# Kernel optimization log

Measured on AMD Instinct MI355X. Metric: run time of the kernel, lower is better.

The kernel has to match this reference:

```python
import jax, jax.numpy as jnp
import numpy as np

N, M, E, DIM, H = 50000, 50000, 640000, 128, 8
DH = DIM // H
EPS = 1e-5

def _prelu(x, alpha):
    return jnp.where(x >= 0, x, alpha * x)

def setup_inputs() -> dict:
    key0 = jax.random.key(0)
    ks = jax.random.split(key0, 12)
    s = 1.0 / np.sqrt(DIM)
    return {
        "query": jax.random.normal(ks[0], (N, DIM), jnp.float32),
        "key": jax.random.normal(ks[1], (M, DIM), jnp.float32),
        "value": jax.random.normal(ks[2], (M, DIM), jnp.float32),
        "query_idx": jax.random.randint(ks[3], (E,), 0, N),
        "key_idx": jax.random.randint(ks[4], (E,), 0, M),
        "Wq": jax.random.normal(ks[5], (DIM, DIM), jnp.float32) * s,
        "bq": jnp.zeros((DIM,), jnp.float32),
        "Wk": jax.random.normal(ks[6], (DIM, DIM), jnp.float32) * s,
        "bk": jnp.zeros((DIM,), jnp.float32),
        "Wv": jax.random.normal(ks[7], (DIM, DIM), jnp.float32) * s,
        "bv": jnp.zeros((DIM,), jnp.float32),
        "Wp": jax.random.normal(ks[8], (DIM, DIM), jnp.float32) * s,
        "bp": jnp.zeros((DIM,), jnp.float32),
        "a": jax.random.normal(ks[9], (1, H, DH), jnp.float32) * 0.1,
        "alpha": jnp.full((1,), 0.25, jnp.float32),
        "gamma": jnp.ones((DIM,), jnp.float32),
        "beta": jnp.zeros((DIM,), jnp.float32),
    }

def reference(query, key, value, query_idx, key_idx, Wq, bq, Wk, bk, Wv, bv, Wp, bp, a, alpha, gamma, beta):
    n = query.shape[0]
    # projections (node-level, then gather per edge; linear commutes with gather)
    Qq = query @ Wq + bq            # [N, DIM]
    Kq = query @ Wk + bk            # [N, DIM] (self-attn key)
    Kk = key @ Wk + bk              # [M, DIM]
    Vq = query @ Wv + bv            # [N, DIM]
    Vv = value @ Wv + bv            # [M, DIM]
    # self-attention score per query node: [N, H, 1]
    attn_qq = (a * _prelu(Qq + Kq, alpha).reshape(n, H, DH)).sum(-1, keepdims=True)
    # per-edge additive attention score: [E, H, 1]
    e_feat = _prelu(Qq[query_idx] + Kk[key_idx], alpha)
    attn_e = (a * e_feat.reshape(-1, H, DH)).sum(-1, keepdims=True)
    # stable softmax over irregular query groups (include self)
    max_attn = jax.lax.stop_gradient(attn_qq.at[query_idx].max(attn_e))
    exp_qq = jnp.exp(attn_qq - max_attn)                 # [N, H, 1]
    exp_e = jnp.exp(attn_e - max_attn[query_idx])        # [E, H, 1]
    denom = exp_qq.at[query_idx].add(exp_e)              # [N, H, 1]
    denom = jnp.where(denom == 0, 1.0, denom)
    # weighted value scatter-sum (value_idx == key_idx)
    msg = exp_qq * Vq.reshape(n, H, DH)
    msg = msg.at[query_idx].add(exp_e * Vv[key_idx].reshape(-1, H, DH))
    out = (msg / denom).reshape(n, DIM) @ Wp + bp
    res = query + out
    mu = res.mean(-1, keepdims=True)
    var = res.var(-1, keepdims=True)
    return gamma * (res - mu) / jnp.sqrt(var + EPS) + beta
```

## Files before the change

kernel.cpp:

```cpp
#include <hip/hip_runtime.h>
#include <math.h>

#define DIM 128
#define NH 8
#define LN_EPS 1e-5f
#define NEGINF -3.0e38f

using bf16x8 = __attribute__((ext_vector_type(8))) short;
using f32x4  = __attribute__((ext_vector_type(4))) float;

__device__ __forceinline__ float prelu_f(float x, float al) { return x >= 0.f ? x : al * x; }

__device__ __forceinline__ short f2bf(float f) {
    unsigned u = __float_as_uint(f);
    unsigned r = (u + 0x7fffu + ((u >> 16) & 1u)) >> 16;
    return (short)r;
}
__device__ __forceinline__ float bflo(unsigned u) { return __uint_as_float(u << 16); }
__device__ __forceinline__ float bfhi(unsigned u) { return __uint_as_float(u & 0xffff0000u); }

__device__ __forceinline__ unsigned cvt_pk_bf16(float lo, float hi) {
    unsigned r;
    asm("v_cvt_pk_bf16_f32 %0, %1, %2" : "=v"(r) : "v"(lo), "v"(hi));
    return r;
}

__device__ __forceinline__ float swz_xor1(float x) {
    return __int_as_float(__builtin_amdgcn_ds_swizzle(__float_as_int(x), 0x041F));
}
__device__ __forceinline__ float swz_xor2(float x) {
    return __int_as_float(__builtin_amdgcn_ds_swizzle(__float_as_int(x), 0x081F));
}
__device__ __forceinline__ float swz_xor16(float x) {
    return __int_as_float(__builtin_amdgcn_ds_swizzle(__float_as_int(x), 0x401F));
}
__device__ __forceinline__ float swz_xor32(float x) {
    return __shfl_xor(x, 32);
}

__global__ __launch_bounds__(256) void setup_kernel(
    const float* __restrict__ W0, const float* __restrict__ W1,
    const float* __restrict__ W2, const float* __restrict__ W3,
    short* __restrict__ P0, short* __restrict__ P1,
    short* __restrict__ P2, short* __restrict__ P3,
    const int* __restrict__ qidx, int* __restrict__ counts, int E)
{
    if (blockIdx.x < 32) {
        const int id = blockIdx.x * 256 + threadIdx.x;
        const int mat = id >> 11;
        const int rem = id & 2047;
        const int ks = rem >> 9;
        const int ct = (rem >> 6) & 7;
        const int lane = rem & 63;
        const int lr = lane & 15, lg = lane >> 4;
        const float* W = mat == 0 ? W0 : mat == 1 ? W1 : mat == 2 ? W2 : W3;
        short* P = mat == 0 ? P0 : mat == 1 ? P1 : mat == 2 ? P2 : P3;
        short v[8];
        #pragma unroll
        for (int r = 0; r < 8; ++r)
            v[r] = f2bf(W[(ks * 32 + lg * 8 + r) * DIM + ct * 16 + lr]);
        *(bf16x8*)&P[(size_t)((ks * 8 + ct) * 64 + lane) * 8] = *(bf16x8*)v;
    } else {
        const int b = blockIdx.x - 32;
        for (int e = b * 256 + threadIdx.x; e < E; e += 1024 * 256)
            atomicAdd(&counts[qidx[e]], 1);
    }
}

__global__ __launch_bounds__(256) void proj_all_mfma(
    const float* __restrict__ query,
    const float* __restrict__ key, const float* __restrict__ value,
    const short* __restrict__ Wqp, const short* __restrict__ Wkp, const short* __restrict__ Wvp,
    const float* __restrict__ bq, const float* __restrict__ bk, const float* __restrict__ bv,
    const float* __restrict__ avec, const float* __restrict__ alpha_p,
    short* __restrict__ QV16, float* __restrict__ attnqq4,
    short* __restrict__ KV16, int N, int M, int nb)
{
    __shared__ unsigned lds[4][16][66];
    const int wid = threadIdx.x >> 6, lane = threadIdx.x & 63;
    const int lr = lane & 15, lg = lane >> 4;
    const bool evenlane = (lane & 1) == 0;

    if ((int)blockIdx.x < nb) {
        const int row0 = ((int)blockIdx.x * 4 + wid) * 16;
        if (row0 >= N) return;
        const int arow = row0 + lr;
        const bool rowok = arow < N;

        bf16x8 afrag[4];
        #pragma unroll
        for (int ks = 0; ks < 4; ++ks) {
            float t[8] = {0.f,0.f,0.f,0.f,0.f,0.f,0.f,0.f};
            if (rowok) {
                *(float4*)&t[0] = *(const float4*)&query[(size_t)arow * DIM + ks * 32 + lg * 8];
                *(float4*)&t[4] = *(const float4*)&query[(size_t)arow * DIM + ks * 32 + lg * 8 + 4];
            }
            union { bf16x8 v; unsigned u[4]; } a;
            a.u[0] = cvt_pk_bf16(t[0], t[1]);
            a.u[1] = cvt_pk_bf16(t[2], t[3]);
            a.u[2] = cvt_pk_bf16(t[4], t[5]);
            a.u[3] = cvt_pk_bf16(t[6], t[7]);
            afrag[ks] = a.v;
        }
        const float al = alpha_p[0];
        unsigned* qvout = (unsigned*)QV16;

        #pragma unroll 2
        for (int ct = 0; ct < 8; ++ct) {
            f32x4 aq = (f32x4)0.f, ak = (f32x4)0.f;
            #pragma unroll
            for (int ks = 0; ks < 4; ++ks) {
                const size_t bo = (size_t)((ks * 8 + ct) * 64 + lane) * 8;
                aq = __builtin_amdgcn_mfma_f32_16x16x32_bf16(afrag[ks], *(const bf16x8*)&Wqp[bo], aq, 0, 0, 0);
                ak = __builtin_amdgcn_mfma_f32_16x16x32_bf16(afrag[ks], *(const bf16x8*)&Wkp[bo], ak, 0, 0, 0);
            }
            const int col = ct * 16 + lr;
            const float bqv = bq[col], bkv = bk[col], av = avec[col];
            #pragma unroll
            for (int r = 0; r < 4; ++r) {
                const int row = lg * 4 + r;
                const float qv = aq[r] + bqv;
                const float kv = ak[r] + bkv;
                float part = av * prelu_f(qv + kv, al);
                part += swz_xor1(part);
                part += swz_xor2(part);
                const int grow = row0 + row;
                if ((lr & 3) == 0 && grow < N)
                    attnqq4[(size_t)grow * 32 + ct * 4 + (lr >> 2)] = part;
                const float qn = swz_xor1(qv);
                if (evenlane) lds[wid][row][ct * 8 + (lr >> 1)] = cvt_pk_bf16(qv, qn);
            }
        }
        #pragma unroll
        for (int rr = 0; rr < 16; ++rr) {
            const int grow = row0 + rr;
            if (grow < N) qvout[(size_t)grow * 128 + lane] = lds[wid][rr][lane];
        }

        #pragma unroll 2
        for (int ct = 0; ct < 8; ++ct) {
            f32x4 acv = (f32x4)0.f;
            #pragma unroll
            for (int ks = 0; ks < 4; ++ks) {
                const size_t bo = (size_t)((ks * 8 + ct) * 64 + lane) * 8;
                acv = __builtin_amdgcn_mfma_f32_16x16x32_bf16(afrag[ks], *(const bf16x8*)&Wvp[bo], acv, 0, 0, 0);
            }
            const int col = ct * 16 + lr;
            const float bvv = bv[col];
            #pragma unroll
            for (int r = 0; r < 4; ++r) {
                const int row = lg * 4 + r;
                const float vv = acv[r] + bvv;
                const float vn = swz_xor1(vv);
                if (evenlane) lds[wid][row][ct * 8 + (lr >> 1)] = cvt_pk_bf16(vv, vn);
            }
        }
        #pragma unroll
        for (int rr = 0; rr < 16; ++rr) {
            const int grow = row0 + rr;
            if (grow < N) qvout[(size_t)grow * 128 + 64 + lane] = lds[wid][rr][lane];
        }
    } else {
        const int row0 = (((int)blockIdx.x - nb) * 4 + wid) * 16;
        if (row0 >= M) return;
        const int arow = row0 + lr;
        const bool rowok = arow < M;
        unsigned* kvout = (unsigned*)KV16;

        {
            bf16x8 afK[4];
            #pragma unroll
            for (int ks = 0; ks < 4; ++ks) {
                float t[8] = {0.f,0.f,0.f,0.f,0.f,0.f,0.f,0.f};
                if (rowok) {
                    *(float4*)&t[0] = *(const float4*)&key[(size_t)arow * DIM + ks * 32 + lg * 8];
                    *(float4*)&t[4] = *(const float4*)&key[(size_t)arow * DIM + ks * 32 + lg * 8 + 4];
                }
                union { bf16x8 v; unsigned u[4]; } a;
                a.u[0] = cvt_pk_bf16(t[0], t[1]);
                a.u[1] = cvt_pk_bf16(t[2], t[3]);
                a.u[2] = cvt_pk_bf16(t[4], t[5]);
                a.u[3] = cvt_pk_bf16(t[6], t[7]);
                afK[ks] = a.v;
            }
            #pragma unroll 2
            for (int ct = 0; ct < 8; ++ct) {
                f32x4 ack = (f32x4)0.f;
                #pragma unroll
                for (int ks = 0; ks < 4; ++ks) {
                    const size_t bo = (size_t)((ks * 8 + ct) * 64 + lane) * 8;
                    ack = __builtin_amdgcn_mfma_f32_16x16x32_bf16(afK[ks], *(const bf16x8*)&Wkp[bo], ack, 0, 0, 0);
                }
                const int col = ct * 16 + lr;
                const float bkv = bk[col];
                #pragma unroll
                for (int r = 0; r < 4; ++r) {
                    const int row = lg * 4 + r;
                    const float kv = ack[r] + bkv;
                    const float kn = swz_xor1(kv);
                    if (evenlane) lds[wid][row][ct * 8 + (lr >> 1)] = cvt_pk_bf16(kv, kn);
                }
            }
            #pragma unroll
            for (int rr = 0; rr < 16; ++rr) {
                const int grow = row0 + rr;
                if (grow < M) kvout[(size_t)grow * 128 + lane] = lds[wid][rr][lane];
            }
        }
        {
            bf16x8 afV[4];
            #pragma unroll
            for (int ks = 0; ks < 4; ++ks) {
                float t[8] = {0.f,0.f,0.f,0.f,0.f,0.f,0.f,0.f};
                if (rowok) {
                    *(float4*)&t[0] = *(const float4*)&value[(size_t)arow * DIM + ks * 32 + lg * 8];
                    *(float4*)&t[4] = *(const float4*)&value[(size_t)arow * DIM + ks * 32 + lg * 8 + 4];
                }
                union { bf16x8 v; unsigned u[4]; } a;
                a.u[0] = cvt_pk_bf16(t[0], t[1]);
                a.u[1] = cvt_pk_bf16(t[2], t[3]);
                a.u[2] = cvt_pk_bf16(t[4], t[5]);
                a.u[3] = cvt_pk_bf16(t[6], t[7]);
                afV[ks] = a.v;
            }
            #pragma unroll 2
            for (int ct = 0; ct < 8; ++ct) {
                f32x4 acv = (f32x4)0.f;
                #pragma unroll
                for (int ks = 0; ks < 4; ++ks) {
                    const size_t bo = (size_t)((ks * 8 + ct) * 64 + lane) * 8;
                    acv = __builtin_amdgcn_mfma_f32_16x16x32_bf16(afV[ks], *(const bf16x8*)&Wvp[bo], acv, 0, 0, 0);
                }
                const int col = ct * 16 + lr;
                const float bvv = bv[col];
                #pragma unroll
                for (int r = 0; r < 4; ++r) {
                    const int row = lg * 4 + r;
                    const float vv = acv[r] + bvv;
                    const float vn = swz_xor1(vv);
                    if (evenlane) lds[wid][row][ct * 8 + (lr >> 1)] = cvt_pk_bf16(vv, vn);
                }
            }
            #pragma unroll
            for (int rr = 0; rr < 16; ++rr) {
                const int grow = row0 + rr;
                if (grow < M) kvout[(size_t)grow * 128 + 64 + lane] = lds[wid][rr][lane];
            }
        }
    }
}

__global__ __launch_bounds__(256) void scan1_kernel(const int* __restrict__ counts,
                                                    int* __restrict__ bsum, int N)
{
    __shared__ int sh[256];
    int i = blockIdx.x * 256 + threadIdx.x;
    sh[threadIdx.x] = (i < N) ? counts[i] : 0;
    __syncthreads();
    #pragma unroll
    for (int off = 128; off; off >>= 1) {
        if (threadIdx.x < off) sh[threadIdx.x] += sh[threadIdx.x + off];
        __syncthreads();
    }
    if (threadIdx.x == 0) bsum[blockIdx.x] = sh[0];
}

__global__ __launch_bounds__(256) void scan2_kernel(const int* __restrict__ bsum,
                                                    int* __restrict__ boff, int B)
{
    int t = threadIdx.x;
    if (B > 256) {
        if (t == 0) { int run = 0; for (int i = 0; i < B; ++i) { int v = bsum[i]; boff[i] = run; run += v; } }
        return;
    }
    __shared__ int sh[256];
    int v = (t < B) ? bsum[t] : 0;
    sh[t] = v;
    __syncthreads();
    for (int off = 1; off < 256; off <<= 1) {
        int x = (t >= off) ? sh[t - off] : 0;
        __syncthreads();
        sh[t] += x;
        __syncthreads();
    }
    if (t < B) boff[t] = sh[t] - v;
}

__global__ __launch_bounds__(256) void scan3_kernel(const int* __restrict__ counts,
                                                    const int* __restrict__ boff,
                                                    int* __restrict__ offsets,
                                                    int* __restrict__ cursor,
                                                    int N, int E)
{
    __shared__ int sh[256];
    int t = threadIdx.x;
    int i = blockIdx.x * 256 + t;
    int v = (i < N) ? counts[i] : 0;
    sh[t] = v;
    __syncthreads();
    for (int off = 1; off < 256; off <<= 1) {
        int x = (t >= off) ? sh[t - off] : 0;
        __syncthreads();
        sh[t] += x;
        __syncthreads();
    }
    int base = boff[blockIdx.x];
    if (i < N) {
        int o = base + sh[t] - v;
        offsets[i] = o;
        cursor[i] = o;
    }
    if (i == 0) offsets[N] = E;
}

__global__ void fill_kernel(const int* __restrict__ qidx, const int* __restrict__ kidx,
                            int* __restrict__ cursor, int* __restrict__ ksorted, int E)
{
    for (int e = blockIdx.x * blockDim.x + threadIdx.x; e < E; e += gridDim.x * blockDim.x) {
        int q = qidx[e];
        int pos = atomicAdd(&cursor[q], 1);
        ksorted[pos] = kidx[e];
    }
}

__global__ __launch_bounds__(256) void edge_agg_kernel(
    const short* __restrict__ QV16, const float* __restrict__ attnqq4,
    const short* __restrict__ KV16,
    const int* __restrict__ ksorted, const int* __restrict__ offsets,
    const float* __restrict__ avec, const float* __restrict__ alpha_p,
    short* __restrict__ msgn16, int N)
{
    const int lane = threadIdx.x & 63;
    const int wid  = threadIdx.x >> 6;
    const int e    = lane >> 4;
    const int sub  = lane & 15;
    const int h    = sub >> 1;

    const float al = alpha_p[0];
    const float r  = (1.f - al) / (1.f + al);
    const float s1 = (1.f + al) * 0.5f;

    float c[8];
    {
        const float4 a0 = *(const float4*)&avec[sub * 8];
        const float4 a1 = *(const float4*)&avec[sub * 8 + 4];
        c[0] = a0.x * s1; c[1] = a0.y * s1; c[2] = a0.z * s1; c[3] = a0.w * s1;
        c[4] = a1.x * s1; c[5] = a1.y * s1; c[6] = a1.z * s1; c[7] = a1.w * s1;
    }

    const int wavesTotal = gridDim.x * 4;

    for (int n = blockIdx.x * 4 + wid; n < N; n += wavesTotal) {
        float q[8];
        {
            unsigned qd[4];
            *(uint4*)qd = *(const uint4*)&QV16[(size_t)n * 256 + sub * 8];
            #pragma unroll
            for (int j = 0; j < 4; ++j) { q[2*j] = bflo(qd[j]); q[2*j+1] = bfhi(qd[j]); }
        }

        float acc[8];
        float den;
        if (e == 0) {
            unsigned vdi[4];
            *(uint4*)vdi = *(const uint4*)&QV16[(size_t)n * 256 + 128 + sub * 8];
            #pragma unroll
            for (int j = 0; j < 4; ++j) { acc[2*j] = bflo(vdi[j]); acc[2*j+1] = bfhi(vdi[j]); }
            den = 1.f;
        } else {
            #pragma unroll
            for (int d = 0; d < 8; ++d) acc[d] = 0.f;
            den = 0.f;
        }

        float m;
        {
            const float4 a4 = *(const float4*)&attnqq4[(size_t)n * 32 + h * 4];
            m = (a4.x + a4.y) + (a4.z + a4.w);
        }

        const int p0 = offsets[n];
        const int p1 = offsets[n + 1];
        bool div = false;

        const int idx0 = p0 + e;
        bool v0 = idx0 < p1;
        const int ki0 = v0 ? ksorted[idx0] : 0;
        unsigned kd0[4], vd0[4];
        {
            const size_t kb = (size_t)ki0 * 256 + sub * 8;
            *(uint4*)kd0 = *(const uint4*)&KV16[kb];
            *(uint4*)vd0 = *(const uint4*)&KV16[kb + 128];
        }

        for (int it = 1; __any(v0); ++it) {
            const int nidx = p0 + it * 4 + e;
            const bool v1 = nidx < p1;
            const int ki1 = v1 ? ksorted[nidx] : 0;
            unsigned kd1[4], vd1[4];
            {
                const size_t kb = (size_t)ki1 * 256 + sub * 8;
                *(uint4*)kd1 = *(const uint4*)&KV16[kb];
                *(uint4*)vd1 = *(const uint4*)&KV16[kb + 128];
            }

            float sp = 0.f;
            #pragma unroll
            for (int j = 0; j < 4; ++j) {
                const float x0 = q[2*j]   + bflo(kd0[j]);
                const float x1 = q[2*j+1] + bfhi(kd0[j]);
                const float t0 = fmaf(r, __builtin_fabsf(x0), x0);
                const float t1 = fmaf(r, __builtin_fabsf(x1), x1);
                sp = fmaf(c[2*j], t0, sp);
                sp = fmaf(c[2*j+1], t1, sp);
            }
            const float sf = sp + swz_xor1(sp);
            const float s = v0 ? sf : NEGINF;
            const float d_ = s - m;

            if (__any(d_ > 8.f)) {
                div = true;
                const float nm = fmaxf(m, s);
                const float cc = __expf(m - nm);
                const float w = __expf(s - nm);
                den = den * cc + w;
                #pragma unroll
                for (int j = 0; j < 4; ++j) {
                    acc[2*j]   = fmaf(acc[2*j],   cc, w * bflo(vd0[j]));
                    acc[2*j+1] = fmaf(acc[2*j+1], cc, w * bfhi(vd0[j]));
                }
                m = nm;
            } else {
                const float w = __expf(d_);
                den += w;
                #pragma unroll
                for (int j = 0; j < 4; ++j) {
                    acc[2*j]   = fmaf(w, bflo(vd0[j]), acc[2*j]);
                    acc[2*j+1] = fmaf(w, bfhi(vd0[j]), acc[2*j+1]);
                }
            }

            #pragma unroll
            for (int j = 0; j < 4; ++j) { kd0[j] = kd1[j]; vd0[j] = vd1[j]; }
            v0 = v1;
        }

        #define MERGE_ROUND(SWZ)                                    \
            {                                                       \
                const float m2 = SWZ(m);                            \
                const float den2 = SWZ(den);                        \
                const float nm = fmaxf(m, m2);                      \
                const float ca = __expf(m - nm);                    \
                const float cb = __expf(m2 - nm);                   \
                den = den * ca + den2 * cb;                         \
                _Pragma("unroll")                                   \
                for (int d = 0; d < 8; ++d)                         \
                    acc[d] = acc[d] * ca + SWZ(acc[d]) * cb;        \
                m = nm;                                             \
            }
        #define SUM_ROUND(SWZ)                                      \
            {                                                       \
                den += SWZ(den);                                    \
                _Pragma("unroll")                                   \
                for (int d = 0; d < 8; ++d) acc[d] += SWZ(acc[d]);  \
            }
        if (div) {
            MERGE_ROUND(swz_xor16);
            MERGE_ROUND(swz_xor32);
        } else {
            SUM_ROUND(swz_xor16);
            SUM_ROUND(swz_xor32);
        }
        #undef MERGE_ROUND
        #undef SUM_ROUND

        if (e == 0) {
            const float inv = 1.f / den;
            unsigned u[4];
            #pragma unroll
            for (int j = 0; j < 4; ++j)
                u[j] = cvt_pk_bf16(acc[2*j] * inv, acc[2*j+1] * inv);
            *(uint4*)&msgn16[(size_t)n * DIM + sub * 8] = *(uint4*)u;
        }
    }
}

__global__ __launch_bounds__(256) void out_ln_mfma(
    const short* __restrict__ msgn16, const short* __restrict__ Wpp,
    const float* __restrict__ bp, const float* __restrict__ query,
    const float* __restrict__ gamma, const float* __restrict__ beta,
    float* __restrict__ out, int N)
{
    __shared__ float ys[64][130];
    const int wid = threadIdx.x >> 6, lane = threadIdx.x & 63;
    const int rowbase = blockIdx.x * 64;
    const int row0 = rowbase + wid * 16;
    const int lr = lane & 15, lg = lane >> 4;

    if (row0 < N) {
        bf16x8 afrag[4];
        const int arow = row0 + lr;
        const bool rowok = arow < N;
        #pragma unroll
        for (int ks = 0; ks < 4; ++ks) {
            if (rowok)
                afrag[ks] = *(const bf16x8*)&msgn16[(size_t)arow * DIM + ks * 32 + lg * 8];
            else {
                bf16x8 z;
                #pragma unroll
                for (int j = 0; j < 8; ++j) z[j] = 0;
                afrag[ks] = z;
            }
        }
        #pragma unroll 2
        for (int ct = 0; ct < 8; ++ct) {
            f32x4 acc = (f32x4)0.f;
            #pragma unroll
            for (int ks = 0; ks < 4; ++ks) {
                const size_t bo = (size_t)((ks * 8 + ct) * 64 + lane) * 8;
                acc = __builtin_amdgcn_mfma_f32_16x16x32_bf16(afrag[ks], *(const bf16x8*)&Wpp[bo], acc, 0, 0, 0);
            }
            const int col = ct * 16 + lr;
            const float bpv = bp[col];
            #pragma unroll
            for (int r = 0; r < 4; ++r)
                ys[wid * 16 + lg * 4 + r][col] = acc[r] + bpv;
        }
    }
    __syncthreads();

    for (int rr = 0; rr < 16; ++rr) {
        const int r = wid * 16 + rr;
        const int grow = rowbase + r;
        if (grow >= N) break;
        const float y1 = ys[r][lane], y2 = ys[r][lane + 64];
        const float q1 = query[(size_t)grow * DIM + lane];
        const float q2 = query[(size_t)grow * DIM + lane + 64];
        const float r1 = y1 + q1, r2 = y2 + q2;
        float s = r1 + r2;
        float ss = r1 * r1 + r2 * r2;
        #pragma unroll
        for (int off = 32; off; off >>= 1) {
            s += __shfl_xor(s, off);
            ss += __shfl_xor(ss, off);
        }
        const float mu = s * (1.f / DIM);
        const float var = ss * (1.f / DIM) - mu * mu;
        const float rstd = rsqrtf(var + LN_EPS);
        out[(size_t)grow * DIM + lane] = gamma[lane] * (r1 - mu) * rstd + beta[lane];
        out[(size_t)grow * DIM + lane + 64] = gamma[lane + 64] * (r2 - mu) * rstd + beta[lane + 64];
    }
}

extern "C" void kernel_launch(void* const* d_in, const int* in_sizes, int n_in,
                              void* d_out, int out_size, void* d_ws, size_t ws_size,
                              hipStream_t stream) {
    const float* query = (const float*)d_in[0];
    const float* key   = (const float*)d_in[1];
    const float* value = (const float*)d_in[2];
    const int* query_idx = (const int*)d_in[3];
    const int* key_idx   = (const int*)d_in[4];
    const float* Wq = (const float*)d_in[5];
    const float* bq = (const float*)d_in[6];
    const float* Wk = (const float*)d_in[7];
    const float* bk = (const float*)d_in[8];
    const float* Wv = (const float*)d_in[9];
    const float* bv = (const float*)d_in[10];
    const float* Wp = (const float*)d_in[11];
    const float* bp = (const float*)d_in[12];
    const float* avec  = (const float*)d_in[13];
    const float* alpha = (const float*)d_in[14];
    const float* gamma = (const float*)d_in[15];
    const float* beta  = (const float*)d_in[16];
    float* out = (float*)d_out;

    const int N = in_sizes[0] / DIM;
    const int M = in_sizes[1] / DIM;
    const int E = in_sizes[3];

    float* f = (float*)d_ws;
    float* attnqq4 = f; f += (size_t)N * 32;
    short* sp = (short*)f;
    short* QV16 = sp;   sp += (size_t)N * 256;
    short* KV16 = sp;   sp += (size_t)M * 256;
    short* msgn16 = sp; sp += (size_t)N * DIM;
    short* Wqp = sp;    sp += DIM * DIM;
    short* Wkp = sp;    sp += DIM * DIM;
    short* Wvp = sp;    sp += DIM * DIM;
    short* Wpp = sp;    sp += DIM * DIM;
    int* ip = (int*)(((size_t)sp + 15) & ~(size_t)15);
    int* counts  = ip;  ip += N;
    int* offsets = ip;  ip += N + 1;
    int* cursor  = ip;  ip += N;
    int* bsum    = ip;  ip += 4096;
    int* boff    = ip;  ip += 4096;
    int* ksorted = ip;  ip += E;

    const int B = (N + 255) / 256;
    const int nb = (N + 63) / 64;
    const int mb = (M + 63) / 64;

    hipMemsetAsync(counts, 0, (size_t)N * sizeof(int), stream);

    setup_kernel<<<1056, 256, 0, stream>>>(Wq, Wk, Wv, Wp, Wqp, Wkp, Wvp, Wpp,
                                           query_idx, counts, E);

    scan1_kernel<<<B, 256, 0, stream>>>(counts, bsum, N);
    scan2_kernel<<<1, 256, 0, stream>>>(bsum, boff, B);
    scan3_kernel<<<B, 256, 0, stream>>>(counts, boff, offsets, cursor, N, E);
    fill_kernel<<<1024, 256, 0, stream>>>(query_idx, key_idx, cursor, ksorted, E);

    proj_all_mfma<<<nb + mb, 256, 0, stream>>>(
        query, key, value, Wqp, Wkp, Wvp, bq, bk, bv, avec, alpha,
        QV16, attnqq4, KV16, N, M, nb);

    edge_agg_kernel<<<2048, 256, 0, stream>>>(
        QV16, attnqq4, KV16, ksorted, offsets, avec, alpha, msgn16, N);

    out_ln_mfma<<<(N + 63) / 64, 256, 0, stream>>>(
        msgn16, Wpp, bp, query, gamma, beta, out, N);
}
```

Baseline: 214.9 us.

## Deepen edge gather pipeline to four in-flight rows with index prefetch

Replaces the single-stage double-buffered edge loop with a four-slot rotating pipeline. Key/value rows for four upcoming edges stay in flight, and the key indices for the batch after that are prefetched. The aim is to hide gather latency on the irregular KV reads and to break the dependent index-then-row load chain. In exchange it raises register pressure, which may lower occupancy, and short neighbor lists waste loads on padded slots.

```diff
diff --git a/kernel.cpp b/kernel.cpp
--- a/kernel.cpp
+++ b/kernel.cpp
@@ -381,69 +381,95 @@
 
         const int p0 = offsets[n];
         const int p1 = offsets[n + 1];
+        const int T  = (p1 - p0 + 3) >> 2;
         bool div = false;
 
-        const int idx0 = p0 + e;
-        bool v0 = idx0 < p1;
-        const int ki0 = v0 ? ksorted[idx0] : 0;
-        unsigned kd0[4], vd0[4];
+        #define ROWLOAD(kd_, vd_, ki_)                                        \
+            {                                                                 \
+                const size_t kb = (size_t)(ki_) * 256 + sub * 8;              \
+                *(uint4*)(kd_) = *(const uint4*)&KV16[kb];                    \
+                *(uint4*)(vd_) = *(const uint4*)&KV16[kb + 128];              \
+            }
+
+        unsigned kdA[4], vdA[4], kdB[4], vdB[4];
+        unsigned kdC[4], vdC[4], kdD[4], vdD[4];
+        bool vA, vB, vC, vD;
+        int kiA, kiB, kiC, kiD;
+
         {
-            const size_t kb = (size_t)ki0 * 256 + sub * 8;
-            *(uint4*)kd0 = *(const uint4*)&KV16[kb];
-            *(uint4*)vd0 = *(const uint4*)&KV16[kb + 128];
-        }
-
-        for (int it = 1; __any(v0); ++it) {
-            const int nidx = p0 + it * 4 + e;
-            const bool v1 = nidx < p1;
-            const int ki1 = v1 ? ksorted[nidx] : 0;
-            unsigned kd1[4], vd1[4];
-            {
-                const size_t kb = (size_t)ki1 * 256 + sub * 8;
-                *(uint4*)kd1 = *(const uint4*)&KV16[kb];
-                *(uint4*)vd1 = *(const uint4*)&KV16[kb + 128];
-            }
-
-            float sp = 0.f;
-            #pragma unroll
-            for (int j = 0; j < 4; ++j) {
-                const float x0 = q[2*j]   + bflo(kd0[j]);
-                const float x1 = q[2*j+1] + bfhi(kd0[j]);
-                const float t0 = fmaf(r, __builtin_fabsf(x0), x0);
-                const float t1 = fmaf(r, __builtin_fabsf(x1), x1);
-                sp = fmaf(c[2*j], t0, sp);
-                sp = fmaf(c[2*j+1], t1, sp);
-            }
-            const float sf = sp + swz_xor1(sp);
-            const float s = v0 ? sf : NEGINF;
-            const float d_ = s - m;
-
-            if (__any(d_ > 8.f)) {
-                div = true;
-                const float nm = fmaxf(m, s);
-                const float cc = __expf(m - nm);
-                const float w = __expf(s - nm);
-                den = den * cc + w;
-                #pragma unroll
-                for (int j = 0; j < 4; ++j) {
-                    acc[2*j]   = fmaf(acc[2*j],   cc, w * bflo(vd0[j]));
-                    acc[2*j+1] = fmaf(acc[2*j+1], cc, w * bfhi(vd0[j]));
-                }
-                m = nm;
-            } else {
-                const float w = __expf(d_);
-                den += w;
-                #pragma unroll
-                for (int j = 0; j < 4; ++j) {
-                    acc[2*j]   = fmaf(w, bflo(vd0[j]), acc[2*j]);
-                    acc[2*j+1] = fmaf(w, bfhi(vd0[j]), acc[2*j+1]);
-                }
-            }
-
-            #pragma unroll
-            for (int j = 0; j < 4; ++j) { kd0[j] = kd1[j]; vd0[j] = vd1[j]; }
-            v0 = v1;
-        }
+            int i0 = p0 + e,      i1 = p0 + 4 + e;
+            int i2 = p0 + 8 + e,  i3 = p0 + 12 + e;
+            vA = i0 < p1; vB = i1 < p1; vC = i2 < p1; vD = i3 < p1;
+            const int k0 = vA ? ksorted[i0] : 0;
+            const int k1 = vB ? ksorted[i1] : 0;
+            const int k2 = vC ? ksorted[i2] : 0;
+            const int k3 = vD ? ksorted[i3] : 0;
+            ROWLOAD(kdA, vdA, k0); ROWLOAD(kdB, vdB, k1);
+            ROWLOAD(kdC, vdC, k2); ROWLOAD(kdD, vdD, k3);
+            int j0 = p0 + 16 + e, j1 = p0 + 20 + e;
+            int j2 = p0 + 24 + e, j3 = p0 + 28 + e;
+            kiA = (j0 < p1) ? ksorted[j0] : 0;
+            kiB = (j1 < p1) ? ksorted[j1] : 0;
+            kiC = (j2 < p1) ? ksorted[j2] : 0;
+            kiD = (j3 < p1) ? ksorted[j3] : 0;
+        }
+
+        #define COMPUTE(kd_, vd_, vflag)                                      \
+            {                                                                 \
+                float sp = 0.f;                                               \
+                _Pragma("unroll")                                             \
+                for (int j = 0; j < 4; ++j) {                                 \
+                    const float x0 = q[2*j]   + bflo(kd_[j]);                 \
+                    const float x1 = q[2*j+1] + bfhi(kd_[j]);                 \
+                    const float t0 = fmaf(r, __builtin_fabsf(x0), x0);        \
+                    const float t1 = fmaf(r, __builtin_fabsf(x1), x1);        \
+                    sp = fmaf(c[2*j], t0, sp);                                \
+                    sp = fmaf(c[2*j+1], t1, sp);                              \
+                }                                                             \
+                const float sf = sp + swz_xor1(sp);                           \
+                const float s = (vflag) ? sf : NEGINF;                        \
+                const float d_ = s - m;                                       \
+                if (__any(d_ > 8.f)) {                                        \
+                    div = true;                                               \
+                    const float nm = fmaxf(m, s);                             \
+                    const float cc = __expf(m - nm);                          \
+                    const float w = __expf(s - nm);                           \
+                    den = den * cc + w;                                       \
+                    _Pragma("unroll")                                         \
+                    for (int j = 0; j < 4; ++j) {                             \
+                        acc[2*j]   = fmaf(acc[2*j],   cc, w * bflo(vd_[j])); \
+                        acc[2*j+1] = fmaf(acc[2*j+1], cc, w * bfhi(vd_[j])); \
+                    }                                                         \
+                    m = nm;                                                   \
+                } else {                                                      \
+                    const float w = __expf(d_);                               \
+                    den += w;                                                 \
+                    _Pragma("unroll")                                         \
+                    for (int j = 0; j < 4; ++j) {                             \
+                        acc[2*j]   = fmaf(w, bflo(vd_[j]), acc[2*j]);         \
+                        acc[2*j+1] = fmaf(w, bfhi(vd_[j]), acc[2*j+1]);       \
+                    }                                                         \
+                }                                                             \
+            }
+
+        #define RELOAD(kd_, vd_, vflag, ki_, st4, st8)                        \
+            {                                                                 \
+                vflag = (p0 + (st4) * 4 + e) < p1;                            \
+                ROWLOAD(kd_, vd_, ki_);                                       \
+                const int fi = p0 + (st8) * 4 + e;                            \
+                ki_ = (fi < p1) ? ksorted[fi] : 0;                            \
+            }
+
+        #pragma unroll 1
+        for (int t = 0; t < T; t += 4) {
+            COMPUTE(kdA, vdA, vA); RELOAD(kdA, vdA, vA, kiA, t + 4, t + 8);
+            COMPUTE(kdB, vdB, vB); RELOAD(kdB, vdB, vB, kiB, t + 5, t + 9);
+            COMPUTE(kdC, vdC, vC); RELOAD(kdC, vdC, vC, kiC, t + 6, t + 10);
+            COMPUTE(kdD, vdD, vD); RELOAD(kdD, vdD, vD, kiD, t + 7, t + 11);
+        }
+        #undef COMPUTE
+        #undef RELOAD
+        #undef ROWLOAD
 
         #define MERGE_ROUND(SWZ)                                    \
             {                                                       \
```

New measurement: 205.6 us. 4.3% less time.
